# Kernel tuning notes

Hardware: AMD Instinct MI355X
Metric: run time of the kernel (lower is better)

Reference implementation:

```python
import jax, jax.numpy as jnp
import numpy as np

B, L, DL, DM, K = 8192, 1, 1024, 1024, 8


def setup_inputs() -> dict:
    key = jax.random.key(0)
    ks = jax.random.split(key, 8)
    s = lambda k, shape, sc=1.0: jax.random.normal(k, shape, jnp.float32) * sc
    return {
        "l_hidden": s(ks[0], (B, L, DL)),
        "m_hidden": s(ks[1], (B, L, DM)),
        "G_l_m": s(ks[2], (DL, K, DM)),   # randn'd each fwd in torch; exposed as input
        "G_m_l": s(ks[3], (DM, K, DL)),
        "l_fc1_w": s(ks[4], (256, DL), 0.02),
        "l_fc1_b": jnp.zeros((256,), jnp.float32),
        "l_fc2_w": s(ks[5], (DL, 256), 0.02),
        "l_fc2_b": jnp.zeros((DL,), jnp.float32),
        "m_fc1_w": s(ks[6], (128, DM), 0.02),
        "m_fc1_b": jnp.zeros((128,), jnp.float32),
        "m_fc2_w": s(ks[7], (DM, 128), 0.02),
        "m_fc2_b": jnp.zeros((DM,), jnp.float32),
    }


def _cross(h_a, h_b, G, g_vec):
    """One direction of the cross-share unit.
    h_a: [B,L,Da], h_b: [B,L,Db], G: [Da,K,Db], g_vec: [B,L,Da]. L must be 1.
    Broadcasts G over batch instead of torch's .repeat (same math, no 256GB copy).
    """
    b, l, da = h_a.shape
    k = G.shape[1]
    # l_hidden @ reshape(G, [Da, K*Db]) -> reshape to [B, L*K, Db]
    s = jnp.einsum('bld,dke->blke', h_a, G).reshape(b, l * k, -1)      # [B,L*K,Db]
    # tanh( shared @ h_b^T ) -> [B, L*K, L]
    t = jnp.tanh(jnp.einsum('bke,bse->bks', s, h_b))                    # [B,L*K,L]
    # reshape [B,L,K,L] -> permute [B,L,L,K] -> [B,L*L,K]
    t = t.reshape(b, l, k, l).transpose(0, 1, 3, 2).reshape(b, l * l, k)
    g = jnp.tile(g_vec, (1, k, 1))                                      # [B,L*K,Da] (L=1 -> [B,K,Da])
    vec = jnp.matmul(t, g)                                              # [B,L*L,Da]
    attn = jax.nn.softmax(vec, axis=-1)
    out = h_a + attn * h_a
    return out, attn


def reference(l_hidden, m_hidden, G_l_m, G_m_l,
              l_fc1_w, l_fc1_b, l_fc2_w, l_fc2_b,
              m_fc1_w, m_fc1_b, m_fc2_w, m_fc2_b):
    # dropout(0.3) is identity in eval mode
    G_vec_l = (l_hidden @ l_fc1_w.T + l_fc1_b) @ l_fc2_w.T + l_fc2_b   # [B,L,DL]
    G_vec_m = (m_hidden @ m_fc1_w.T + m_fc1_b) @ m_fc2_w.T + m_fc2_b   # [B,L,DM]
    l_out, l_attn = _cross(l_hidden, m_hidden, G_l_m, G_vec_l)
    m_out, m_attn = _cross(m_hidden, l_hidden, G_m_l, G_vec_m)
    return l_out, m_out, l_attn, m_attn
```

## Files before the change

### kernel.cpp

```cpp
#include <hip/hip_runtime.h>


#define NB 8192
#define DD 1024

typedef __bf16 bf16x8 __attribute__((ext_vector_type(8)));
typedef float f32x4 __attribute__((ext_vector_type(4)));

__device__ __forceinline__ unsigned short f2bf(float f) {
  unsigned u = __float_as_uint(f);
  u += 0x7FFFu + ((u >> 16) & 1u);
  return (unsigned short)(u >> 16);
}
__device__ __forceinline__ float bf2f(unsigned short h) {
  return __uint_as_float(((unsigned)h) << 16);
}

__global__ __launch_bounds__(256) void split_cast_k(
    const float* __restrict__ in, unsigned short* __restrict__ hi,
    unsigned short* __restrict__ lo, int n4) {
  int i = blockIdx.x * 256 + threadIdx.x;
  if (i >= n4) return;
  float4 v = reinterpret_cast<const float4*>(in)[i];
  float vv[4] = {v.x, v.y, v.z, v.w};
  unsigned short hh[4], ll[4];
#pragma unroll
  for (int c = 0; c < 4; ++c) {
    hh[c] = f2bf(vv[c]);
    ll[c] = f2bf(vv[c] - bf2f(hh[c]));
  }
  reinterpret_cast<ushort4*>(hi)[i] = make_ushort4(hh[0], hh[1], hh[2], hh[3]);
  reinterpret_cast<ushort4*>(lo)[i] = make_ushort4(ll[0], ll[1], ll[2], ll[3]);
}

__global__ __launch_bounds__(256) void transpose_split_k(
    const float* __restrict__ G, unsigned short* __restrict__ bhi,
    unsigned short* __restrict__ blo) {
  __shared__ float t[32][33];
  int c0 = blockIdx.x * 32;
  int d0 = blockIdx.y * 32;
  int tx = threadIdx.x & 31;
  int tg = threadIdx.x >> 5;
#pragma unroll
  for (int s = 0; s < 4; ++s) {
    int dr = tg * 4 + s;
    t[dr][tx] = G[(size_t)(d0 + dr) * 8192 + c0 + tx];
  }
  __syncthreads();
#pragma unroll
  for (int s = 0; s < 4; ++s) {
    int cr = tg * 4 + s;
    float v = t[tx][cr];
    size_t o = (size_t)(c0 + cr) * 1024 + d0 + tx;
    unsigned short h = f2bf(v);
    bhi[o] = h;
    blo[o] = f2bf(v - bf2f(h));
  }
}

__global__ __launch_bounds__(256) void wct_k(
    const float* __restrict__ w1, const float* __restrict__ b1,
    const float* __restrict__ w2, const float* __restrict__ b2, int J,
    unsigned short* __restrict__ bhi, unsigned short* __restrict__ blo,
    float* __restrict__ bc) {
  __shared__ float w2row[256];
  int n = blockIdx.x;
  int tid = threadIdx.x;
  if (tid < J) w2row[tid] = w2[n * J + tid];
  __syncthreads();
#pragma unroll
  for (int s = 0; s < 4; ++s) {
    int i = tid + s * 256;
    float acc = 0.f;
    for (int j = 0; j < J; ++j) acc = fmaf(w2row[j], w1[j * 1024 + i], acc);
    size_t o = (size_t)(8192 + n) * 1024 + i;
    unsigned short h = f2bf(acc);
    bhi[o] = h;
    blo[o] = f2bf(acc - bf2f(h));
  }
  if (tid == 0) {
    float acc = 0.f;
    for (int j = 0; j < J; ++j) acc = fmaf(w2row[j], b1[j], acc);
    bc[n] = acc + b2[n];
  }
}

#define SBAR() do { asm volatile("" ::: "memory"); __builtin_amdgcn_s_barrier(); asm volatile("" ::: "memory"); } while (0)
#define WAITV2() asm volatile("s_waitcnt vmcnt(2)" ::: "memory")

__global__ __launch_bounds__(512, 2) void gemm_k(
    const unsigned short* __restrict__ Ahi_, const unsigned short* __restrict__ Alo_,
    const unsigned short* __restrict__ Bhi_, const unsigned short* __restrict__ Blo_,
    const float* __restrict__ hb, float* __restrict__ gvec, float* __restrict__ x) {
  __shared__ __align__(16) char lds[147456];
  const char* Ah = (const char*)Ahi_;
  const char* Al = (const char*)Alo_;
  const char* Bh = (const char*)Bhi_;
  const char* Bl = (const char*)Blo_;

  const int tid = threadIdx.x;
  const int lane = tid & 63;
  const int wid = tid >> 6;
  const int wm = wid >> 2, wn = wid & 3;

  const int bid = blockIdx.x;
  const int wg = (bid & 7) * 144 + (bid >> 3);
  const int by = wg & 31;
  const int bx = wg >> 5;
  const int m0 = by * 256, n0 = bx * 256;
  const int nt = (n0 >= 8192) ? 16 : 48;
  const int nt4 = nt * 4;

  const int rowl = tid >> 3;
  const int colsw = ((tid & 7) ^ ((tid >> 3) & 7)) << 4;
  const int rowb = (lane & 15) << 7;
  const int s0 = ((lane >> 4) ^ (lane & 7)) << 4;
  const int s1 = s0 ^ 64;

  f32x4 acc[8][4] = {};

#define GLOAD(SRC, DST)                                              \
  __builtin_amdgcn_global_load_lds(                                  \
      (const __attribute__((address_space(1))) void*)(SRC),          \
      (__attribute__((address_space(3))) void*)(lds + (DST)), 16, 0, 0)

  auto stage = [&](int h) {
    const char* src;
    int dst;
    if (h < nt4) {
      const int th = h >> 2, q = h & 3, seg = th >> 4;
      const char* mat;
      int rowoff;
      if (q < 2) {
        mat = (seg == 1) ? Al : Ah;
        rowoff = m0 + (q & 1) * 128;
        dst = (th & 1) * 32768 + (q & 1) * 16384;
      } else {
        mat = (seg == 2) ? Bl : Bh;
        rowoff = n0 + (q & 1) * 128;
        dst = 65536 + (th & 1) * 32768 + (q & 1) * 16384;
      }
      src = mat + (size_t)(rowoff + rowl) * 2048 + ((th & 15) << 7) + colsw;
    } else {
      src = Ah + (size_t)(m0 + rowl) * 2048 + colsw;
      dst = 131072;
    }
    dst += wid * 1024;
    GLOAD(src, dst);
    GLOAD(src + 64 * 2048, dst + 8192);
  };

  auto ldA = [&](bf16x8 (*d)[2], int msub, int cb) {
#pragma unroll
    for (int f = 0; f < 4; ++f) {
      const char* p = lds + cb + wm * 16384 + msub * 8192 + f * 2048 + rowb;
      d[f][0] = *reinterpret_cast<const bf16x8*>(p + s0);
      d[f][1] = *reinterpret_cast<const bf16x8*>(p + s1);
    }
  };
  auto ldB = [&](bf16x8 (*d)[2], int nsub, int cb) {
#pragma unroll
    for (int g = 0; g < 2; ++g) {
      const char* p = lds + 65536 + cb + wn * 8192 + (nsub * 2 + g) * 2048 + rowb;
      d[g][0] = *reinterpret_cast<const bf16x8*>(p + s0);
      d[g][1] = *reinterpret_cast<const bf16x8*>(p + s1);
    }
  };
  auto mm = [&](int iof, bf16x8 (*aa)[2], int jof, bf16x8 (*bb)[2]) {
#pragma unroll
    for (int f = 0; f < 4; ++f)
#pragma unroll
      for (int g = 0; g < 2; ++g) {
        acc[iof + f][jof + g] = __builtin_amdgcn_mfma_f32_16x16x32_bf16(
            aa[f][0], bb[g][0], acc[iof + f][jof + g], 0, 0, 0);
        acc[iof + f][jof + g] = __builtin_amdgcn_mfma_f32_16x16x32_bf16(
            aa[f][1], bb[g][1], acc[iof + f][jof + g], 0, 0, 0);
      }
  };

  for (int h = 0; h < 5; ++h) stage(h);
  WAITV2();
  SBAR();

  for (int t = 0; t < nt; ++t) {
    const int cb = (t & 1) * 32768;
    bf16x8 af0[4][2], af1[4][2], b0[2][2], b1[2][2];

    ldA(af0, 0, cb);
    ldB(b0, 0, cb);
    stage(4 * t + 5);
    SBAR();
    __builtin_amdgcn_s_setprio(1);
    mm(0, af0, 0, b0);
    __builtin_amdgcn_s_setprio(0);
    SBAR();
    ldB(b1, 1, cb);
    stage(4 * t + 6);
    SBAR();
    __builtin_amdgcn_s_setprio(1);
    mm(0, af0, 2, b1);
    __builtin_amdgcn_s_setprio(0);
    SBAR();
    ldA(af1, 1, cb);
    stage(4 * t + 7);
    SBAR();
    __builtin_amdgcn_s_setprio(1);
    mm(4, af1, 0, b0);
    __builtin_amdgcn_s_setprio(0);
    SBAR();
    stage(4 * t + 8);
    WAITV2();
    SBAR();
    __builtin_amdgcn_s_setprio(1);
    mm(4, af1, 2, b1);
    __builtin_amdgcn_s_setprio(0);
    SBAR();
  }

  const int coll = lane & 15;
  const int rg = (lane >> 4) * 4;
  if (n0 >= 8192) {
#pragma unroll
    for (int i = 0; i < 8; ++i)
#pragma unroll
      for (int r = 0; r < 4; ++r) {
        const int row = m0 + wm * 128 + i * 16 + rg + r;
#pragma unroll
        for (int j = 0; j < 4; ++j) {
          const int gcol = (n0 - 8192) + wn * 64 + j * 16 + coll;
          gvec[(size_t)row * 1024 + gcol] = acc[i][j][r];
        }
      }
  } else {
    const int kidx = n0 >> 10;
    const int ebase = (n0 & 1023) + wn * 64 + coll;
#pragma unroll
    for (int i = 0; i < 8; ++i)
#pragma unroll
      for (int r = 0; r < 4; ++r) {
        const int row = m0 + wm * 128 + i * 16 + rg + r;
        const float* hr = hb + (size_t)row * 1024 + ebase;
        float tmp = acc[i][0][r] * hr[0] + acc[i][1][r] * hr[16] +
                    acc[i][2][r] * hr[32] + acc[i][3][r] * hr[48];
#pragma unroll
        for (int s = 1; s < 16; s <<= 1) tmp += __shfl_xor(tmp, s);
        if (coll == 0) atomicAdd(&x[row * 8 + kidx], tmp);
      }
  }
}

__global__ __launch_bounds__(256) void finalize_k(
    const float* __restrict__ xk, const float* __restrict__ gvec,
    const float* __restrict__ bc, const float* __restrict__ ha,
    float* __restrict__ out, float* __restrict__ attn) {
  int b = blockIdx.x;
  int tid = threadIdx.x;
  float S = 0.f;
#pragma unroll
  for (int k = 0; k < 8; ++k) S += tanhf(xk[b * 8 + k]);
  float v[4];
  float mx = -3.4e38f;
#pragma unroll
  for (int s = 0; s < 4; ++s) {
    int d = tid + s * 256;
    v[s] = S * (gvec[(size_t)b * 1024 + d] + bc[d]);
    mx = fmaxf(mx, v[s]);
  }
  __shared__ float red[8];
#pragma unroll
  for (int off = 32; off >= 1; off >>= 1) mx = fmaxf(mx, __shfl_xor(mx, off));
  int lane = tid & 63, w = tid >> 6;
  if (lane == 0) red[w] = mx;
  __syncthreads();
  float m = fmaxf(fmaxf(red[0], red[1]), fmaxf(red[2], red[3]));
  float e[4], sum = 0.f;
#pragma unroll
  for (int s = 0; s < 4; ++s) { e[s] = __expf(v[s] - m); sum += e[s]; }
#pragma unroll
  for (int off = 32; off >= 1; off >>= 1) sum += __shfl_xor(sum, off);
  if (lane == 0) red[4 + w] = sum;
  __syncthreads();
  float inv = 1.f / (red[4] + red[5] + red[6] + red[7]);
#pragma unroll
  for (int s = 0; s < 4; ++s) {
    int d = tid + s * 256;
    float a = e[s] * inv;
    attn[(size_t)b * 1024 + d] = a;
    float h = ha[(size_t)b * 1024 + d];
    out[(size_t)b * 1024 + d] = fmaf(a, h, h);
  }
}

extern "C" void kernel_launch(void* const* d_in, const int* in_sizes, int n_in,
                              void* d_out, int out_size, void* d_ws, size_t ws_size,
                              hipStream_t stream) {
  const float* l_hidden = (const float*)d_in[0];
  const float* m_hidden = (const float*)d_in[1];
  const float* G_l_m = (const float*)d_in[2];
  const float* G_m_l = (const float*)d_in[3];
  const float* l_fc1_w = (const float*)d_in[4];
  const float* l_fc1_b = (const float*)d_in[5];
  const float* l_fc2_w = (const float*)d_in[6];
  const float* l_fc2_b = (const float*)d_in[7];
  const float* m_fc1_w = (const float*)d_in[8];
  const float* m_fc1_b = (const float*)d_in[9];
  const float* m_fc2_w = (const float*)d_in[10];
  const float* m_fc2_b = (const float*)d_in[11];
  float* out = (float*)d_out;

  char* ws = (char*)d_ws;
  unsigned short* Ahi = (unsigned short*)(ws);
  unsigned short* Alo = (unsigned short*)(ws + 16777216);
  unsigned short* Bhi = (unsigned short*)(ws + 33554432);
  unsigned short* Blo = (unsigned short*)(ws + 52428800);
  float* gvec = (float*)(ws + 71303168);
  float* x = (float*)(ws + 104857600);
  float* bc = (float*)(ws + 105381888);

  hipMemsetAsync(x, 0, 2 * NB * 8 * sizeof(float), stream);

  const size_t BD = (size_t)NB * DD;
  dim3 gemmGrid(1152);

  split_cast_k<<<(int)(BD / 4 / 256), 256, 0, stream>>>(l_hidden, Ahi, Alo, (int)(BD / 4));
  transpose_split_k<<<dim3(256, 32), 256, 0, stream>>>(G_l_m, Bhi, Blo);
  wct_k<<<1024, 256, 0, stream>>>(l_fc1_w, l_fc1_b, l_fc2_w, l_fc2_b, 256, Bhi, Blo, bc);
  gemm_k<<<gemmGrid, 512, 0, stream>>>(Ahi, Alo, Bhi, Blo, m_hidden, gvec, x);
  finalize_k<<<NB, 256, 0, stream>>>(x, gvec, bc, l_hidden, out, out + 2 * BD);

  split_cast_k<<<(int)(BD / 4 / 256), 256, 0, stream>>>(m_hidden, Ahi, Alo, (int)(BD / 4));
  transpose_split_k<<<dim3(256, 32), 256, 0, stream>>>(G_m_l, Bhi, Blo);
  wct_k<<<1024, 256, 0, stream>>>(m_fc1_w, m_fc1_b, m_fc2_w, m_fc2_b, 128, Bhi, Blo, bc);
  gemm_k<<<gemmGrid, 512, 0, stream>>>(Ahi, Alo, Bhi, Blo, l_hidden, gvec, x + NB * 8);
  finalize_k<<<NB, 256, 0, stream>>>(x + NB * 8, gvec, bc, m_hidden, out + BD, out + 3 * BD);
}
```

Before: 1.244 ms.

## Restructure GEMM into quadrant-ordered staging with finer vmcnt waits and XCD-local tiling

Reorganizes the bf16 split GEMM main loop so each 256x256 tile is split into four 128x128 quadrants, each staged and consumed separately. Waits are tightened to vmcnt(6)/vmcnt(4) at several points so compute can start on a quadrant as soon as its data lands. The block-to-tile mapping is also changed so each XCD handles a contiguous group of M rows, aiming for better L2 reuse. The epilogue is rewritten to match the new accumulator layout. The finer waits and reordered loads risk pipeline hazards, and the new mapping may change cache behaviour.

```diff
diff --git a/kernel.cpp b/kernel.cpp
--- a/kernel.cpp
+++ b/kernel.cpp
@@ -86,7 +86,13 @@
 }
 
 #define SBAR() do { asm volatile("" ::: "memory"); __builtin_amdgcn_s_barrier(); asm volatile("" ::: "memory"); } while (0)
-#define WAITV2() asm volatile("s_waitcnt vmcnt(2)" ::: "memory")
+#define WAITV4() asm volatile("s_waitcnt vmcnt(4)" ::: "memory")
+#define WAITV6() asm volatile("s_waitcnt vmcnt(6)" ::: "memory")
+
+#define GLOAD(SRC, DST)                                              \
+  __builtin_amdgcn_global_load_lds(                                  \
+      (const __attribute__((address_space(1))) void*)(SRC),          \
+      (__attribute__((address_space(3))) void*)(lds + (DST)), 16, 0, 0)
 
 __global__ __launch_bounds__(512, 2) void gemm_k(
     const unsigned short* __restrict__ Ahi_, const unsigned short* __restrict__ Alo_,
@@ -104,116 +110,110 @@
   const int wm = wid >> 2, wn = wid & 3;
 
   const int bid = blockIdx.x;
-  const int wg = (bid & 7) * 144 + (bid >> 3);
-  const int by = wg & 31;
-  const int bx = wg >> 5;
+  const int xcd = bid & 7, j = bid >> 3;
+  const int by = xcd * 4 + (j & 3);
+  const int bx = j >> 2;
   const int m0 = by * 256, n0 = bx * 256;
   const int nt = (n0 >= 8192) ? 16 : 48;
-  const int nt4 = nt * 4;
 
   const int rowl = tid >> 3;
   const int colsw = ((tid & 7) ^ ((tid >> 3) & 7)) << 4;
-  const int rowb = (lane & 15) << 7;
   const int s0 = ((lane >> 4) ^ (lane & 7)) << 4;
   const int s1 = s0 ^ 64;
 
-  f32x4 acc[8][4] = {};
-
-#define GLOAD(SRC, DST)                                              \
-  __builtin_amdgcn_global_load_lds(                                  \
-      (const __attribute__((address_space(1))) void*)(SRC),          \
-      (__attribute__((address_space(3))) void*)(lds + (DST)), 16, 0, 0)
-
-  auto stage = [&](int h) {
-    const char* src;
-    int dst;
-    if (h < nt4) {
-      const int th = h >> 2, q = h & 3, seg = th >> 4;
+  f32x4 acc[4][4][2] = {};
+
+  auto stage = [&](int tile, int q) {
+    if (tile < nt) {
+      const int seg = tile >> 4;
       const char* mat;
-      int rowoff;
+      int rowbase, dst;
       if (q < 2) {
         mat = (seg == 1) ? Al : Ah;
-        rowoff = m0 + (q & 1) * 128;
-        dst = (th & 1) * 32768 + (q & 1) * 16384;
+        rowbase = m0 + q * 128;
+        dst = (tile & 1) * 32768 + q * 16384;
       } else {
         mat = (seg == 2) ? Bl : Bh;
-        rowoff = n0 + (q & 1) * 128;
-        dst = 65536 + (th & 1) * 32768 + (q & 1) * 16384;
+        rowbase = n0 + (q - 2) * 128;
+        dst = 65536 + (tile & 1) * 32768 + (q - 2) * 16384;
       }
-      src = mat + (size_t)(rowoff + rowl) * 2048 + ((th & 15) << 7) + colsw;
+      const char* src = mat + (size_t)(rowbase + rowl) * 2048 + ((tile & 15) << 7) + colsw;
+      dst += wid * 1024;
+      GLOAD(src, dst);
+      GLOAD(src + 64 * 2048, dst + 8192);
     } else {
-      src = Ah + (size_t)(m0 + rowl) * 2048 + colsw;
-      dst = 131072;
-    }
-    dst += wid * 1024;
-    GLOAD(src, dst);
-    GLOAD(src + 64 * 2048, dst + 8192);
+      const char* src = Ah + (size_t)(m0 + rowl) * 2048 + colsw;
+      const int d2 = 131072 + wid * 1024;
+      GLOAD(src, d2);
+      GLOAD(src + 64 * 2048, d2 + 8192);
+    }
   };
 
-  auto ldA = [&](bf16x8 (*d)[2], int msub, int cb) {
+  auto ldA = [&](bf16x8 (*d)[2], int qa, int cb) {
+    const char* p = lds + cb + qa * 16384 + (wm * 64 + (lane & 15)) * 128;
 #pragma unroll
     for (int f = 0; f < 4; ++f) {
-      const char* p = lds + cb + wm * 16384 + msub * 8192 + f * 2048 + rowb;
-      d[f][0] = *reinterpret_cast<const bf16x8*>(p + s0);
-      d[f][1] = *reinterpret_cast<const bf16x8*>(p + s1);
+      d[f][0] = *reinterpret_cast<const bf16x8*>(p + f * 2048 + s0);
+      d[f][1] = *reinterpret_cast<const bf16x8*>(p + f * 2048 + s1);
     }
   };
-  auto ldB = [&](bf16x8 (*d)[2], int nsub, int cb) {
+  auto ldB = [&](bf16x8 (*d)[2], int qb, int cb) {
+    const char* p = lds + 65536 + cb + qb * 16384 + (wn * 32 + (lane & 15)) * 128;
 #pragma unroll
     for (int g = 0; g < 2; ++g) {
-      const char* p = lds + 65536 + cb + wn * 8192 + (nsub * 2 + g) * 2048 + rowb;
-      d[g][0] = *reinterpret_cast<const bf16x8*>(p + s0);
-      d[g][1] = *reinterpret_cast<const bf16x8*>(p + s1);
+      d[g][0] = *reinterpret_cast<const bf16x8*>(p + g * 2048 + s0);
+      d[g][1] = *reinterpret_cast<const bf16x8*>(p + g * 2048 + s1);
     }
   };
-  auto mm = [&](int iof, bf16x8 (*aa)[2], int jof, bf16x8 (*bb)[2]) {
+  auto mm = [&](f32x4 (*ac)[2], bf16x8 (*aa)[2], bf16x8 (*bb)[2]) {
 #pragma unroll
     for (int f = 0; f < 4; ++f)
 #pragma unroll
       for (int g = 0; g < 2; ++g) {
-        acc[iof + f][jof + g] = __builtin_amdgcn_mfma_f32_16x16x32_bf16(
-            aa[f][0], bb[g][0], acc[iof + f][jof + g], 0, 0, 0);
-        acc[iof + f][jof + g] = __builtin_amdgcn_mfma_f32_16x16x32_bf16(
-            aa[f][1], bb[g][1], acc[iof + f][jof + g], 0, 0, 0);
+        ac[f][g] = __builtin_amdgcn_mfma_f32_16x16x32_bf16(aa[f][0], bb[g][0], ac[f][g], 0, 0, 0);
+        ac[f][g] = __builtin_amdgcn_mfma_f32_16x16x32_bf16(aa[f][1], bb[g][1], ac[f][g], 0, 0, 0);
       }
   };
 
-  for (int h = 0; h < 5; ++h) stage(h);
-  WAITV2();
+  stage(0, 0); stage(0, 2);
+  stage(0, 3);
+  stage(0, 1);
+  WAITV4();
   SBAR();
 
+  bf16x8 af[4][2], af2[4][2], bv[2][2], bv2[2][2];
   for (int t = 0; t < nt; ++t) {
     const int cb = (t & 1) * 32768;
-    bf16x8 af0[4][2], af1[4][2], b0[2][2], b1[2][2];
-
-    ldA(af0, 0, cb);
-    ldB(b0, 0, cb);
-    stage(4 * t + 5);
+    ldA(af, 0, cb);
+    ldB(bv, 0, cb);
+    stage(t + 1, 0); stage(t + 1, 2);
     SBAR();
     __builtin_amdgcn_s_setprio(1);
-    mm(0, af0, 0, b0);
+    mm(acc[0], af, bv);
     __builtin_amdgcn_s_setprio(0);
-    SBAR();
-    ldB(b1, 1, cb);
-    stage(4 * t + 6);
+    WAITV6();
+    SBAR();
+    ldB(bv2, 1, cb);
+    stage(t + 1, 3);
     SBAR();
     __builtin_amdgcn_s_setprio(1);
-    mm(0, af0, 2, b1);
+    mm(acc[1], af, bv2);
     __builtin_amdgcn_s_setprio(0);
-    SBAR();
-    ldA(af1, 1, cb);
-    stage(4 * t + 7);
+    WAITV6();
+    SBAR();
+    ldA(af2, 1, cb);
+    stage(t + 1, 1);
     SBAR();
     __builtin_amdgcn_s_setprio(1);
-    mm(4, af1, 0, b0);
+    mm(acc[2], af2, bv2);
     __builtin_amdgcn_s_setprio(0);
     SBAR();
-    stage(4 * t + 8);
-    WAITV2();
+    ldB(bv, 0, cb);
     SBAR();
     __builtin_amdgcn_s_setprio(1);
-    mm(4, af1, 2, b1);
+    mm(acc[3], af2, bv);
     __builtin_amdgcn_s_setprio(0);
+    WAITV4();
     SBAR();
   }
 
@@ -221,31 +221,41 @@
   const int rg = (lane >> 4) * 4;
   if (n0 >= 8192) {
 #pragma unroll
-    for (int i = 0; i < 8; ++i)
-#pragma unroll
-      for (int r = 0; r < 4; ++r) {
-        const int row = m0 + wm * 128 + i * 16 + rg + r;
-#pragma unroll
-        for (int j = 0; j < 4; ++j) {
-          const int gcol = (n0 - 8192) + wn * 64 + j * 16 + coll;
-          gvec[(size_t)row * 1024 + gcol] = acc[i][j][r];
+    for (int q = 0; q < 4; ++q) {
+      const int qm = (q >= 2);
+      const int qn = (q == 1 || q == 2);
+#pragma unroll
+      for (int f = 0; f < 4; ++f)
+#pragma unroll
+        for (int r = 0; r < 4; ++r) {
+          const int row = m0 + qm * 128 + wm * 64 + f * 16 + rg + r;
+#pragma unroll
+          for (int g = 0; g < 2; ++g) {
+            const int gcol = (n0 - 8192) + qn * 128 + wn * 32 + g * 16 + coll;
+            gvec[(size_t)row * 1024 + gcol] = acc[q][f][g][r];
+          }
         }
-      }
+    }
   } else {
     const int kidx = n0 >> 10;
-    const int ebase = (n0 & 1023) + wn * 64 + coll;
-#pragma unroll
-    for (int i = 0; i < 8; ++i)
-#pragma unroll
-      for (int r = 0; r < 4; ++r) {
-        const int row = m0 + wm * 128 + i * 16 + rg + r;
-        const float* hr = hb + (size_t)row * 1024 + ebase;
-        float tmp = acc[i][0][r] * hr[0] + acc[i][1][r] * hr[16] +
-                    acc[i][2][r] * hr[32] + acc[i][3][r] * hr[48];
-#pragma unroll
-        for (int s = 1; s < 16; s <<= 1) tmp += __shfl_xor(tmp, s);
-        if (coll == 0) atomicAdd(&x[row * 8 + kidx], tmp);
-      }
+    const int ebase = (n0 & 1023) + wn * 32 + coll;
+#pragma unroll
+    for (int qm = 0; qm < 2; ++qm) {
+      f32x4 (*acA)[2] = acc[qm ? 3 : 0];
+      f32x4 (*acB)[2] = acc[qm ? 2 : 1];
+#pragma unroll
+      for (int f = 0; f < 4; ++f)
+#pragma unroll
+        for (int r = 0; r < 4; ++r) {
+          const int row = m0 + qm * 128 + wm * 64 + f * 16 + rg + r;
+          const float* hr = hb + (size_t)row * 1024 + ebase;
+          float tmp = acA[f][0][r] * hr[0] + acA[f][1][r] * hr[16] +
+                      acB[f][0][r] * hr[128] + acB[f][1][r] * hr[144];
+#pragma unroll
+          for (int s = 1; s < 16; s <<= 1) tmp += __shfl_xor(tmp, s);
+          if (coll == 0) atomicAdd(&x[row * 8 + kidx], tmp);
+        }
+    }
   }
 }
 
```

Result: faster. 1.095 ms (-12.0%).
